# Optimization experiments

Measured on AMD Instinct MI355X. Metric: run time of the kernel, lower is better.

Reference implementation:

```python
import jax, jax.numpy as jnp
import numpy as np

EPS = 1e-5


def mish(x):
    return x * jnp.tanh(jax.nn.softplus(x))


def layer_norm(x, g, b):
    mu = jnp.mean(x, axis=-1, keepdims=True)
    var = jnp.var(x, axis=-1, keepdims=True)
    return (x - mu) / jnp.sqrt(var + EPS) * g + b


def setup_inputs() -> dict:
    key = jax.random.key(0)
    ks = jax.random.split(key, 10)
    D = 256      # hidden_size == encoder feature dim
    L = 64       # max_length
    B, N, K, Q = 2, 10, 1, 5
    NQ = N * Q   # na_rate = 0
    s = 0.02
    inp = {
        "support": jax.random.normal(ks[0], (B * N * K, L, D), jnp.float32),
        "query": jax.random.normal(ks[1], (B * NQ, L, D), jnp.float32),
        "ln_g": jnp.ones((D,), jnp.float32),
        "ln_b": jnp.zeros((D,), jnp.float32),
        "ln2_g": jnp.ones((2 * D,), jnp.float32),
        "ln2_b": jnp.zeros((2 * D,), jnp.float32),
        "proj_W": jax.random.normal(ks[2], (D, 4 * D), jnp.float32) * s,
        "proj_b": jnp.zeros((D,), jnp.float32),
        "W1": jax.random.normal(ks[3], (D, 4 * D), jnp.float32) * s,
        "b1": jnp.zeros((D,), jnp.float32),
        "W2": jax.random.normal(ks[4], (1, D), jnp.float32) * s,
        "b2": jnp.zeros((1,), jnp.float32),
        "W3": jax.random.normal(ks[5], (1, 1), jnp.float32) * s,  # MLP_out Linear(K=1, 1)
        "b3": jnp.zeros((1,), jnp.float32),
        "N": N, "K": K, "Q": Q,
    }
    return inp


def reference(support, query, ln_g, ln_b, ln2_g, ln2_b, proj_W, proj_b,
              W1, b1, W2, b2, W3, b3, N, K, Q):
    L, D = support.shape[-2], support.shape[-1]
    B = support.shape[0] // (N * K)
    NQ = query.shape[0] // B  # = N*Q + na*Q

    s = layer_norm(support, ln_g, ln_b)
    q = layer_norm(query, ln_g, ln_b)

    # expand to all (query, support) pairs: [B, NQ, N*K, L, D] -> [M, L, D]
    s_e = jnp.broadcast_to(s.reshape(B, 1, N * K, L, D), (B, NQ, N * K, L, D)).reshape(-1, L, D)
    q_e = jnp.broadcast_to(q.reshape(B, NQ, 1, L, D), (B, NQ, N * K, L, D)).reshape(-1, L, D)

    # bidirectional cross-attention (no scaling, as in the original)
    att = jnp.einsum('mld,mkd->mlk', s_e, q_e)            # [M, Ls, Lq]
    s_att = jnp.einsum('mlk,mkd->mld', jax.nn.softmax(att, axis=2), q_e)
    q_att = jnp.einsum('mlk,mld->mkd', jax.nn.softmax(att, axis=1), s_e)

    enh_s = jnp.concatenate([s_e, s_att, jnp.abs(s_e - s_att), s_e * s_att], axis=-1)
    enh_q = jnp.concatenate([q_e, q_att, jnp.abs(q_e - q_att), q_e * q_att], axis=-1)
    s_p = mish(enh_s @ proj_W.T + proj_b)
    q_p = mish(enh_q @ proj_W.T + proj_b)

    # pool_norm: max+mean over length, then LayerNorm(2D)
    s_pool = layer_norm(jnp.concatenate([jnp.max(s_p, axis=-2), jnp.mean(s_p, axis=-2)], axis=-1), ln2_g, ln2_b)
    q_pool = layer_norm(jnp.concatenate([jnp.max(q_p, axis=-2), jnp.mean(q_p, axis=-2)], axis=-1), ln2_g, ln2_b)

    cat_seq = jnp.concatenate([q_pool, s_pool], axis=-1)  # [M, 4D]
    h = mish(cat_seq @ W1.T + b1) @ W2.T + b2             # MLProc -> [M, 1]
    logits = mish(h) @ W3.T + b3                          # MLP_out (K=1) -> [M, 1]

    logits = logits.reshape(B, NQ, N)
    minn = jnp.min(logits, axis=-1)
    logits = jnp.concatenate([logits, minn[..., None] - 1.0], axis=2)  # [B, NQ, N+1]
    pred = jnp.argmax(logits.reshape(-1, N + 1), axis=1)
    return logits, pred
```

## Files before the change

### kernel.cpp

```cpp
#include <hip/hip_runtime.h>

typedef unsigned int u32;
typedef unsigned short u16;
#define LN_EPS 1e-5f

typedef __attribute__((ext_vector_type(8))) short short8v;
typedef __attribute__((ext_vector_type(4))) float f32x4;

#define MFMA(acc, a, b) acc = __builtin_amdgcn_mfma_f32_16x16x32_bf16(a, b, acc, 0, 0, 0)

__device__ __forceinline__ float wave_sum(float v){
  #pragma unroll
  for (int o = 32; o > 0; o >>= 1) v += __shfl_xor(v, o, 64);
  return v;
}
__device__ __forceinline__ float mishf(float v){
  float t = __expf(v);
  float u = t*t + 2.f*t;
  return v * (1.f - 2.f/(u + 2.f));
}
__device__ __forceinline__ float bf2f(u16 h){
  return __uint_as_float(((u32)h) << 16);
}
__device__ __forceinline__ u32 pack_split(float x){
  u32 u = __float_as_uint(x);
  u32 h = (u + 0x8000u) & 0xffff0000u;
  float lf = x - __uint_as_float(h);
  return h | (__float_as_uint(lf) >> 16);
}
__device__ __forceinline__ void split_pair(float x0, float x1, u32& hw, u32& lw){
  u32 u0 = __float_as_uint(x0), u1 = __float_as_uint(x1);
  u32 h0 = (u0 + 0x8000u) & 0xffff0000u;
  u32 h1 = (u1 + 0x8000u) & 0xffff0000u;
  float l0 = x0 - __uint_as_float(h0);
  float l1 = x1 - __uint_as_float(h1);
  hw = (h0 >> 16) | h1;
  lw = (__float_as_uint(l0) >> 16) | (__float_as_uint(l1) & 0xffff0000u);
}
__device__ __forceinline__ void split8v(f32x4 a, f32x4 b, short8v& hi, short8v& lo){
  union { short8v v; u32 w[4]; } H, L;
  split_pair(a[0], a[1], H.w[0], L.w[0]);
  split_pair(a[2], a[3], H.w[1], L.w[1]);
  split_pair(b[0], b[1], H.w[2], L.w[2]);
  split_pair(b[2], b[3], H.w[3], L.w[3]);
  hi = H.v; lo = L.v;
}
__device__ __forceinline__ void unpack8(uint4 q0, uint4 q1, short8v& hi, short8v& lo){
  union { short8v v; u32 w[4]; } H, L;
  H.w[0] = (q0.x >> 16) | (q0.y & 0xffff0000u);
  L.w[0] = (q0.x & 0xffffu) | (q0.y << 16);
  H.w[1] = (q0.z >> 16) | (q0.w & 0xffff0000u);
  L.w[1] = (q0.z & 0xffffu) | (q0.w << 16);
  H.w[2] = (q1.x >> 16) | (q1.y & 0xffff0000u);
  L.w[2] = (q1.x & 0xffffu) | (q1.y << 16);
  H.w[3] = (q1.z >> 16) | (q1.w & 0xffff0000u);
  L.w[3] = (q1.z & 0xffffu) | (q1.w << 16);
  hi = H.v; lo = L.v;
}

__global__ void k_setup_ln(const float* __restrict__ sup, const float* __restrict__ qry,
                           const float* __restrict__ lng, const float* __restrict__ lnb,
                           u16* __restrict__ SHI, u16* __restrict__ SLO,
                           u16* __restrict__ QHI, u16* __restrict__ QLO)
{
  const int seq = blockIdx.x;
  const float* src; u16 *dh, *dl;
  if (seq < 20){
    src = sup + (size_t)seq*16384;
    dh = SHI + (size_t)seq*16384; dl = SLO + (size_t)seq*16384;
  } else {
    src = qry + (size_t)(seq-20)*16384;
    dh = QHI + (size_t)(seq-20)*16384; dl = QLO + (size_t)(seq-20)*16384;
  }
  const int t = threadIdx.x, w = t >> 6, lane = t & 63;
  float4 g4 = *(const float4*)(lng + lane*4);
  float4 b4 = *(const float4*)(lnb + lane*4);
  for (int r = w; r < 64; r += 4){
    float4 x = *(const float4*)(src + r*256 + lane*4);
    float s  = wave_sum(x.x + x.y + x.z + x.w);
    float sq = wave_sum(x.x*x.x + x.y*x.y + x.z*x.z + x.w*x.w);
    float mu = s*(1.f/256.f);
    float rstd = 1.f/sqrtf(sq*(1.f/256.f) - mu*mu + LN_EPS);
    float y0 = (x.x - mu)*rstd*g4.x + b4.x;
    float y1 = (x.y - mu)*rstd*g4.y + b4.y;
    float y2 = (x.z - mu)*rstd*g4.z + b4.z;
    float y3 = (x.w - mu)*rstd*g4.w + b4.w;
    u32 p0 = pack_split(y0), p1 = pack_split(y1), p2 = pack_split(y2), p3 = pack_split(y3);
    ushort4 hv = make_ushort4((u16)(p0>>16),(u16)(p1>>16),(u16)(p2>>16),(u16)(p3>>16));
    ushort4 lv = make_ushort4((u16)(p0&0xffffu),(u16)(p1&0xffffu),(u16)(p2&0xffffu),(u16)(p3&0xffffu));
    *(ushort4*)(dh + r*256 + lane*4) = hv;
    *(ushort4*)(dl + r*256 + lane*4) = lv;
  }
}

__global__ void k_setup_w(const float* __restrict__ Wg,
                          u16* __restrict__ WHI, u16* __restrict__ WLO)
{
  const int gid = blockIdx.x*256 + threadIdx.x;
  const int ks = gid >> 10, rem = gid & 1023, nt = rem >> 6, l = rem & 63;
  const int n  = nt*16 + (l & 15);
  const int k0 = ks*32 + (l >> 4)*8;
  const float* src = Wg + n*1024 + k0;
  float4 xa = *(const float4*)src;
  float4 xb = *(const float4*)(src + 4);
  f32x4 fa, fb;
  fa[0]=xa.x; fa[1]=xa.y; fa[2]=xa.z; fa[3]=xa.w;
  fb[0]=xb.x; fb[1]=xb.y; fb[2]=xb.z; fb[3]=xb.w;
  short8v hi, lo;
  split8v(fa, fb, hi, lo);
  *(short8v*)(WHI + (size_t)gid*8) = hi;
  *(short8v*)(WLO + (size_t)gid*8) = lo;
}

__global__ void k_setup_w1t(const float* __restrict__ W1, float* __restrict__ W1T2)
{
  const int gid = blockIdx.x*256 + threadIdx.x;
  const int kb = gid >> 8, n = gid & 255;
  float4 v = *(const float4*)(W1 + n*1024 + kb*4);
  *(float4*)(W1T2 + kb*1024 + n*4) = v;
}

__global__ __launch_bounds__(256) void k_setup_xp(
    const u16* __restrict__ SHI, const u16* __restrict__ SLO,
    const u16* __restrict__ QHI, const u16* __restrict__ QLO,
    const u16* __restrict__ WHI, const u16* __restrict__ WLO,
    float* __restrict__ XPS, float* __restrict__ XPQ)
{
  const int seq = blockIdx.x;
  const u16 *Xh, *Xl; float* out;
  if (seq < 20){
    Xh = SHI + (size_t)seq*16384; Xl = SLO + (size_t)seq*16384;
    out = XPS + (size_t)seq*16384;
  } else {
    Xh = QHI + (size_t)(seq-20)*16384; Xl = QLO + (size_t)(seq-20)*16384;
    out = XPQ + (size_t)(seq-20)*16384;
  }
  const int t = threadIdx.x, w = t >> 6, l = t & 63;
  const int l15 = l & 15, l4 = l >> 4;
  const int Mg = w >> 1, Ng = w & 1;

  f32x4 acc[2][8];
  #pragma unroll
  for (int i = 0; i < 2; i++)
    #pragma unroll
    for (int j = 0; j < 8; j++){ acc[i][j][0]=0.f; acc[i][j][1]=0.f; acc[i][j][2]=0.f; acc[i][j][3]=0.f; }

  for (int ks = 0; ks < 8; ks++){
    short8v ah[2], al[2];
    #pragma unroll
    for (int mt = 0; mt < 2; mt++){
      const int ro = (Mg*32 + mt*16 + l15)*256 + ks*32 + l4*8;
      ah[mt] = *(const short8v*)(Xh + ro);
      al[mt] = *(const short8v*)(Xl + ro);
    }
    #pragma unroll
    for (int nt = 0; nt < 8; nt++){
      const int fo = (ks*16 + Ng*8 + nt)*512 + l*8;
      short8v bh = *(const short8v*)(WHI + fo);
      short8v bl = *(const short8v*)(WLO + fo);
      #pragma unroll
      for (int mt = 0; mt < 2; mt++){
        MFMA(acc[mt][nt], ah[mt], bh);
        MFMA(acc[mt][nt], ah[mt], bl);
        MFMA(acc[mt][nt], al[mt], bh);
      }
    }
  }
  #pragma unroll
  for (int mt = 0; mt < 2; mt++)
    #pragma unroll
    for (int nt = 0; nt < 8; nt++)
      #pragma unroll
      for (int r = 0; r < 4; r++)
        out[(Mg*32 + mt*16 + l4*4 + r)*256 + Ng*128 + nt*16 + l15] = acc[mt][nt][r];
}

#define WLH(BUF, C, H) { const int base_ = (((C)*8 + ch)*16 + Ng*8 + (H)*4)*512 + l*8; \
  _Pragma("unroll") for (int j_ = 0; j_ < 4; j_++){ \
    BUF[j_*2]   = *(const short8v*)(WHI + base_ + j_*512); \
    BUF[j_*2+1] = *(const short8v*)(WLO + base_ + j_*512); } }
#define WMH(BUF, G, H) { _Pragma("unroll") for (int j_ = 0; j_ < 4; j_++){ \
  MFMA(acc[0][(H)*4+j_], fh[G][0], BUF[j_*2]); \
  MFMA(acc[0][(H)*4+j_], fh[G][0], BUF[j_*2+1]); \
  MFMA(acc[0][(H)*4+j_], fl[G][0], BUF[j_*2]); \
  MFMA(acc[1][(H)*4+j_], fh[G][1], BUF[j_*2]); \
  MFMA(acc[1][(H)*4+j_], fh[G][1], BUF[j_*2+1]); \
  MFMA(acc[1][(H)*4+j_], fl[G][1], BUF[j_*2]); } }

__global__ __launch_bounds__(256, 2) void k_pair13(
    const u16* __restrict__ SHI, const u16* __restrict__ SLO,
    const u16* __restrict__ QHI, const u16* __restrict__ QLO,
    const u16* __restrict__ WHI, const u16* __restrict__ WLO,
    const float* __restrict__ XPS, const float* __restrict__ XPQ,
    const float* __restrict__ W1T2,
    const float* __restrict__ pbias,
    const float* __restrict__ ln2g, const float* __restrict__ ln2b,
    const float* __restrict__ b1,
    const float* __restrict__ W2,  const float* __restrict__ b2,
    const float* __restrict__ W3,  const float* __restrict__ b3,
    float* __restrict__ logits)
{
  __shared__ float SM[17296];
  float* S0  = SM;
  u16*   OcT = (u16*)(SM + 4352);
  float* AOc = SM + 9472;
  u32*   P   = (u32*)(SM + 11776);
  float* cat = SM + 16128;
  float* smx = SM + 17152;
  float* smi = SM + 17216;
  float* red = SM + 17280;
  float* stat= SM + 17288;
  float* mred= SM + 17290;

  const int m = (blockIdx.x & 7)*125 + (blockIdx.x >> 3);
  const int b = m / 500, rr = m % 500, nq = rr / 10, n_ = rr % 10;
  const u16* Sh = SHI + (size_t)(b*10 + n_) * 16384;
  const u16* Sl = SLO + (size_t)(b*10 + n_) * 16384;
  const u16* Qh = QHI + (size_t)(b*50 + nq) * 16384;
  const u16* Ql = QLO + (size_t)(b*50 + nq) * 16384;
  const float* xpS = XPS + (size_t)(b*10 + n_) * 16384;
  const float* xpQ = XPQ + (size_t)(b*50 + nq) * 16384;

  const int t = threadIdx.x, w = t >> 6, l = t & 63;
  const int l15 = l & 15, l4 = l >> 4;

  {
    f32x4 acc4[4];
    #pragma unroll
    for (int i = 0; i < 4; i++){ acc4[i][0]=0.f; acc4[i][1]=0.f; acc4[i][2]=0.f; acc4[i][3]=0.f; }
    const u16* Sa = Sh + (w*16+l15)*256 + l4*8;
    const u16* Sb = Sl + (w*16+l15)*256 + l4*8;
    short8v ah = *(const short8v*)Sa;
    short8v al = *(const short8v*)Sb;
    short8v bh[4], bl[4];
    #pragma unroll
    for (int nt = 0; nt < 4; nt++){
      bh[nt] = *(const short8v*)(Qh + (nt*16+l15)*256 + l4*8);
      bl[nt] = *(const short8v*)(Ql + (nt*16+l15)*256 + l4*8);
    }
    #pragma unroll
    for (int ch = 0; ch < 8; ch++){
      short8v nah, nal, nbh[4], nbl[4];
      if (ch < 7){
        nah = *(const short8v*)(Sa + (ch+1)*32);
        nal = *(const short8v*)(Sb + (ch+1)*32);
        #pragma unroll
        for (int nt = 0; nt < 4; nt++){
          nbh[nt] = *(const short8v*)(Qh + (nt*16+l15)*256 + (ch+1)*32 + l4*8);
          nbl[nt] = *(const short8v*)(Ql + (nt*16+l15)*256 + (ch+1)*32 + l4*8);
        }
      }
      #pragma unroll
      for (int nt = 0; nt < 4; nt++){
        MFMA(acc4[nt], ah, bh[nt]);
        MFMA(acc4[nt], ah, bl[nt]);
        MFMA(acc4[nt], al, bh[nt]);
      }
      if (ch < 7){
        ah = nah; al = nal;
        #pragma unroll
        for (int nt = 0; nt < 4; nt++){ bh[nt] = nbh[nt]; bl[nt] = nbl[nt]; }
      }
    }
    #pragma unroll
    for (int nt = 0; nt < 4; nt++)
      #pragma unroll
      for (int r = 0; r < 4; r++)
        S0[(w*16 + l4*4 + r)*68 + nt*16 + l15] = acc4[nt][r];
    __syncthreads();
  }

  auto softmax_row = [&](){
    if (t < 64){
      float mxv = -1e30f, sm = 0.f;
      for (int k = 0; k < 64; k++) mxv = fmaxf(mxv, S0[t*68 + k]);
      for (int k = 0; k < 64; k++) sm += __expf(S0[t*68 + k] - mxv);
      smx[t] = mxv; smi[t] = 1.f/sm;
    }
    __syncthreads();
    #pragma unroll
    for (int r = 0; r < 16; r++){
      int idx = t + 256*r, ll = idx >> 6, k = idx & 63;
      P[ll*68 + k] = pack_split(__expf(S0[ll*68 + k] - smx[ll]) * smi[ll]);
    }
    __syncthreads();
  };
  auto softmax_col_T = [&](){
    if (t < 64){
      float mxv = -1e30f, sm = 0.f;
      for (int ld = 0; ld < 64; ld++) mxv = fmaxf(mxv, S0[ld*68 + t]);
      for (int ld = 0; ld < 64; ld++) sm += __expf(S0[ld*68 + t] - mxv);
      smx[t] = mxv; smi[t] = 1.f/sm;
    }
    __syncthreads();
    #pragma unroll
    for (int r = 0; r < 16; r++){
      int idx = t + 256*r, ll = idx >> 6, k = idx & 63;
      P[k*68 + ll] = pack_split(__expf(S0[ll*68 + k] - smx[k]) * smi[k]);
    }
    __syncthreads();
  };

  auto do_side = [&](const u16* Xh, const u16* Xl, const u16* Oh, const u16* Ol,
                     const float* xp, int cat_off){
    const int Mg = w >> 1, Ng = w & 1;
    f32x4 acc[2][8];
    #pragma unroll
    for (int mt = 0; mt < 2; mt++)
      #pragma unroll
      for (int nt = 0; nt < 8; nt++){
        const float* xr = xp + (Mg*32 + mt*16 + l4*4)*256 + Ng*128 + nt*16 + l15;
        acc[mt][nt][0] = xr[0];
        acc[mt][nt][1] = xr[256];
        acc[mt][nt][2] = xr[512];
        acc[mt][nt][3] = xr[768];
      }

    short8v svh = *(const short8v*)(Oh + l*256 + w*8);
    short8v svl = *(const short8v*)(Ol + l*256 + w*8);
    #pragma unroll
    for (int e = 0; e < 8; e++){
      OcT[(w*8+e)*80 + l]        = (u16)svh[e];
      OcT[2560 + (w*8+e)*80 + l] = (u16)svl[e];
    }
    svh = *(const short8v*)(Oh + l*256 + 32 + w*8);
    svl = *(const short8v*)(Ol + l*256 + 32 + w*8);
    __syncthreads();

    const int xoff = (Mg*32 + l15)*256 + l4*8;

    #pragma unroll 1
    for (int ch = 0; ch < 8; ch++){
      short8v xh0 = *(const short8v*)(Xh + xoff + ch*32);
      short8v xl0 = *(const short8v*)(Xl + xoff + ch*32);
      short8v xh1 = *(const short8v*)(Xh + xoff + 4096 + ch*32);
      short8v xl1 = *(const short8v*)(Xl + xoff + 4096 + ch*32);

      {
        const u16* Ob = OcT + (ch&1)*5120;
        f32x4 ao0 = {0.f,0.f,0.f,0.f}, ao1 = {0.f,0.f,0.f,0.f};
        #pragma unroll
        for (int ks = 0; ks < 2; ks++){
          const u32* pp = P + (w*16 + l15)*68 + ks*32 + l4*8;
          uint4 q0 = *(const uint4*)pp;
          uint4 q1 = *(const uint4*)(pp + 4);
          short8v ph, pl; unpack8(q0, q1, ph, pl);
          const u16* ob0 = Ob + l15*80 + ks*32 + l4*8;
          const u16* ob1 = Ob + (16 + l15)*80 + ks*32 + l4*8;
          short8v bh0 = *(const short8v*)ob0;
          short8v bl0 = *(const short8v*)(ob0 + 2560);
          short8v bh1 = *(const short8v*)ob1;
          short8v bl1 = *(const short8v*)(ob1 + 2560);
          MFMA(ao0, ph, bh0); MFMA(ao0, ph, bl0); MFMA(ao0, pl, bh0);
          MFMA(ao1, ph, bh1); MFMA(ao1, ph, bl1); MFMA(ao1, pl, bh1);
        }
        #pragma unroll
        for (int r = 0; r < 4; r++){
          AOc[(w*16 + l4*4 + r)*36 + l15]      = ao0[r];
          AOc[(w*16 + l4*4 + r)*36 + 16 + l15] = ao1[r];
        }
      }
      __syncthreads();

      if (ch < 7){
        u16* Ob1 = OcT + ((ch+1)&1)*5120;
        #pragma unroll
        for (int e = 0; e < 8; e++){
          Ob1[(w*8+e)*80 + l]        = (u16)svh[e];
          Ob1[2560 + (w*8+e)*80 + l] = (u16)svl[e];
        }
      }
      if (ch < 6){
        svh = *(const short8v*)(Oh + l*256 + (ch+2)*32 + w*8);
        svl = *(const short8v*)(Ol + l*256 + (ch+2)*32 + w*8);
      }

      short8v fh[3][2], fl[3][2];
      {
        f32x4 xv0[2], xv1[2], av0[2], av1[2];
        #pragma unroll
        for (int mt_ = 0; mt_ < 2; mt_++){
          short8v xh = mt_ ? xh1 : xh0;
          short8v xl = mt_ ? xl1 : xl0;
          #pragma unroll
          for (int e_ = 0; e_ < 4; e_++){
            xv0[mt_][e_] = bf2f((u16)xh[e_])     + bf2f((u16)xl[e_]);
            xv1[mt_][e_] = bf2f((u16)xh[4 + e_]) + bf2f((u16)xl[4 + e_]);
          }
          const int row = Mg*32 + mt_*16 + l15;
          av0[mt_] = *(const f32x4*)(AOc + row*36 + l4*8);
          av1[mt_] = *(const f32x4*)(AOc + row*36 + l4*8 + 4);
        }
        #pragma unroll
        for (int mt_ = 0; mt_ < 2; mt_++){
          split8v(av0[mt_], av1[mt_], fh[0][mt_], fl[0][mt_]);
          f32x4 d0, d1, p0, p1;
          #pragma unroll
          for (int e_ = 0; e_ < 4; e_++){
            d0[e_] = fabsf(xv0[mt_][e_] - av0[mt_][e_]);
            d1[e_] = fabsf(xv1[mt_][e_] - av1[mt_][e_]);
            p0[e_] = xv0[mt_][e_] * av0[mt_][e_];
            p1[e_] = xv1[mt_][e_] * av1[mt_][e_];
          }
          split8v(d0, d1, fh[1][mt_], fl[1][mt_]);
          split8v(p0, p1, fh[2][mt_], fl[2][mt_]);
        }
      }

      {
        short8v wa[8], wb[8];
        WLH(wa, 1, 0); WLH(wb, 1, 1);
        WMH(wa, 0, 0);
        WLH(wa, 2, 0);
        WMH(wb, 0, 1);
        WLH(wb, 2, 1);
        WMH(wa, 1, 0);
        WLH(wa, 3, 0);
        WMH(wb, 1, 1);
        WLH(wb, 3, 1);
        WMH(wa, 2, 0);
        WMH(wb, 2, 1);
      }
      __syncthreads();
    }

    float* pmax2 = (float*)P;
    float* psum2 = pmax2 + 512;
    #pragma unroll
    for (int nt = 0; nt < 8; nt++){
      const int col = Ng*128 + nt*16 + l15;
      const float pb = pbias[col];
      float mx = -1e30f, sm = 0.f;
      #pragma unroll
      for (int mt_ = 0; mt_ < 2; mt_++)
        #pragma unroll
        for (int r = 0; r < 4; r++){
          float v = mishf(acc[mt_][nt][r] + pb);
          mx = fmaxf(mx, v); sm += v;
        }
      mx = fmaxf(mx, __shfl_xor(mx, 16, 64));
      mx = fmaxf(mx, __shfl_xor(mx, 32, 64));
      sm += __shfl_xor(sm, 16, 64);
      sm += __shfl_xor(sm, 32, 64);
      if (l4 == 0){ pmax2[Mg*256 + col] = mx; psum2[Mg*256 + col] = sm; }
    }
    __syncthreads();
    float v1 = fmaxf(pmax2[t], pmax2[256 + t]);
    float v2 = (psum2[t] + psum2[256 + t]) * (1.f/64.f);
    float p1 = wave_sum(v1 + v2);
    float p2 = wave_sum(v1*v1 + v2*v2);
    if (l == 0){ red[w] = p1; red[4 + w] = p2; }
    __syncthreads();
    if (t == 0){
      float s1 = red[0]+red[1]+red[2]+red[3];
      float s2 = red[4]+red[5]+red[6]+red[7];
      float mu  = s1 * (1.f/512.f);
      float var = s2 * (1.f/512.f) - mu*mu;
      stat[0] = mu; stat[1] = 1.f/sqrtf(var + LN_EPS);
    }
    __syncthreads();
    float mu = stat[0], rstd = stat[1];
    cat[cat_off + t]       = (v1 - mu)*rstd*ln2g[t]       + ln2b[t];
    cat[cat_off + 256 + t] = (v2 - mu)*rstd*ln2g[256 + t] + ln2b[256 + t];
    __syncthreads();
  };

  softmax_row();
  do_side(Sh, Sl, Qh, Ql, xpS, 512);
  softmax_col_T();
  do_side(Qh, Ql, Sh, Sl, xpQ, 0);

  {
    float acc1 = 0.f;
    const float* wt = W1T2 + t*4;
    #pragma unroll 8
    for (int kb = 0; kb < 256; kb++){
      float4 wv = *(const float4*)(wt + kb*1024);
      const float* cp = &cat[kb*4];
      acc1 += cp[0]*wv.x + cp[1]*wv.y + cp[2]*wv.z + cp[3]*wv.w;
    }
    float hv = mishf(acc1 + b1[t]);
    float contrib = wave_sum(hv * W2[t]);
    if (l == 0) mred[w] = contrib;
  }
  __syncthreads();
  if (t == 0){
    float hh = mred[0] + mred[1] + mred[2] + mred[3] + b2[0];
    logits[m] = mishf(hh)*W3[0] + b3[0];
  }
}

__global__ void k_final9(const float* __restrict__ logits, float* __restrict__ out){
  int t = threadIdx.x;
  if (t < 100){
    float v[10];
    float mn = 1e30f;
    #pragma unroll
    for (int j = 0; j < 10; j++){ v[j] = logits[t*10 + j]; mn = fminf(mn, v[j]); }
    float best = -1e30f; int bi = 0;
    #pragma unroll
    for (int j = 0; j < 10; j++){ if (v[j] > best){ best = v[j]; bi = j; } }
    #pragma unroll
    for (int j = 0; j < 10; j++) out[t*11 + j] = v[j];
    out[t*11 + 10] = mn - 1.f;
    out[1100 + t] = (float)bi;
  }
}

extern "C" void kernel_launch(void* const* d_in, const int* in_sizes, int n_in,
                              void* d_out, int out_size, void* d_ws, size_t ws_size,
                              hipStream_t stream){
  (void)in_sizes; (void)n_in; (void)out_size; (void)ws_size;
  const float* support = (const float*)d_in[0];
  const float* query   = (const float*)d_in[1];
  const float* ln_g    = (const float*)d_in[2];
  const float* ln_b    = (const float*)d_in[3];
  const float* ln2_g   = (const float*)d_in[4];
  const float* ln2_b   = (const float*)d_in[5];
  const float* proj_W  = (const float*)d_in[6];
  const float* proj_b  = (const float*)d_in[7];
  const float* W1      = (const float*)d_in[8];
  const float* b1      = (const float*)d_in[9];
  const float* W2      = (const float*)d_in[10];
  const float* b2      = (const float*)d_in[11];
  const float* W3      = (const float*)d_in[12];
  const float* b3      = (const float*)d_in[13];

  char* wsb = (char*)d_ws;
  float* logits = (float*)wsb;
  u16* SHI = (u16*)(wsb + 4096);
  u16* SLO = SHI + (size_t)20*16384;
  u16* QHI = SLO + (size_t)20*16384;
  u16* QLO = QHI + (size_t)100*16384;
  u16* WHI = QLO + (size_t)100*16384;
  u16* WLO = WHI + (size_t)262144;
  float* XPS  = (float*)(WLO + (size_t)262144);
  float* XPQ  = XPS + (size_t)20*16384;
  float* W1T2 = XPQ + (size_t)100*16384;

  k_setup_ln<<<dim3(120), dim3(256), 0, stream>>>(support, query, ln_g, ln_b,
                                                  SHI, SLO, QHI, QLO);
  k_setup_w<<<dim3(128), dim3(256), 0, stream>>>(proj_W, WHI, WLO);
  k_setup_w1t<<<dim3(256), dim3(256), 0, stream>>>(W1, W1T2);
  k_setup_xp<<<dim3(120), dim3(256), 0, stream>>>(SHI, SLO, QHI, QLO, WHI, WLO,
                                                  XPS, XPQ);
  k_pair13<<<dim3(1000), dim3(256), 0, stream>>>(SHI, SLO, QHI, QLO, WHI, WLO,
                                                 XPS, XPQ, W1T2,
                                                 proj_b, ln2_g, ln2_b,
                                                 b1, W2, b2, W3, b3, logits);
  k_final9<<<dim3(1), dim3(128), 0, stream>>>(logits, (float*)d_out);
}
```

Before: 399.9 us.

## Merge setup kernels and double-buffer attention output to drop a barrier per chunk

Fuses the three setup kernels (LayerNorm split, proj weight split, W1 transpose) into one launch with block-index dispatch. In the main pair kernel, the attention-output staging buffer becomes double-buffered in shared memory. This lets one __syncthreads per chunk be removed and moves the first weight-fragment load earlier so it overlaps the attention MFMA work. The cost is more shared memory per block, which may reduce occupancy, and a longer live range for the weight registers.

Result: no change. 395.5 us, median of 3 (-1.1%).

```diff
diff --git a/kernel.cpp b/kernel.cpp
--- a/kernel.cpp
+++ b/kernel.cpp
@@ -58,66 +58,66 @@
   hi = H.v; lo = L.v;
 }
 
-__global__ void k_setup_ln(const float* __restrict__ sup, const float* __restrict__ qry,
-                           const float* __restrict__ lng, const float* __restrict__ lnb,
-                           u16* __restrict__ SHI, u16* __restrict__ SLO,
-                           u16* __restrict__ QHI, u16* __restrict__ QLO)
+__global__ void k_setup_A(const float* __restrict__ sup, const float* __restrict__ qry,
+                          const float* __restrict__ lng, const float* __restrict__ lnb,
+                          const float* __restrict__ Wg,  const float* __restrict__ W1,
+                          u16* __restrict__ SHI, u16* __restrict__ SLO,
+                          u16* __restrict__ QHI, u16* __restrict__ QLO,
+                          u16* __restrict__ WHI, u16* __restrict__ WLO,
+                          float* __restrict__ W1T2)
 {
-  const int seq = blockIdx.x;
-  const float* src; u16 *dh, *dl;
-  if (seq < 20){
-    src = sup + (size_t)seq*16384;
-    dh = SHI + (size_t)seq*16384; dl = SLO + (size_t)seq*16384;
+  const int bid = blockIdx.x, t = threadIdx.x;
+
+  if (bid < 120){
+    const int seq = bid;
+    const float* src; u16 *dh, *dl;
+    if (seq < 20){
+      src = sup + (size_t)seq*16384;
+      dh = SHI + (size_t)seq*16384; dl = SLO + (size_t)seq*16384;
+    } else {
+      src = qry + (size_t)(seq-20)*16384;
+      dh = QHI + (size_t)(seq-20)*16384; dl = QLO + (size_t)(seq-20)*16384;
+    }
+    const int w = t >> 6, lane = t & 63;
+    float4 g4 = *(const float4*)(lng + lane*4);
+    float4 b4 = *(const float4*)(lnb + lane*4);
+    for (int r = w; r < 64; r += 4){
+      float4 x = *(const float4*)(src + r*256 + lane*4);
+      float s  = wave_sum(x.x + x.y + x.z + x.w);
+      float sq = wave_sum(x.x*x.x + x.y*x.y + x.z*x.z + x.w*x.w);
+      float mu = s*(1.f/256.f);
+      float rstd = 1.f/sqrtf(sq*(1.f/256.f) - mu*mu + LN_EPS);
+      float y0 = (x.x - mu)*rstd*g4.x + b4.x;
+      float y1 = (x.y - mu)*rstd*g4.y + b4.y;
+      float y2 = (x.z - mu)*rstd*g4.z + b4.z;
+      float y3 = (x.w - mu)*rstd*g4.w + b4.w;
+      u32 p0 = pack_split(y0), p1 = pack_split(y1), p2 = pack_split(y2), p3 = pack_split(y3);
+      ushort4 hv = make_ushort4((u16)(p0>>16),(u16)(p1>>16),(u16)(p2>>16),(u16)(p3>>16));
+      ushort4 lv = make_ushort4((u16)(p0&0xffffu),(u16)(p1&0xffffu),(u16)(p2&0xffffu),(u16)(p3&0xffffu));
+      *(ushort4*)(dh + r*256 + lane*4) = hv;
+      *(ushort4*)(dl + r*256 + lane*4) = lv;
+    }
+  } else if (bid < 248){
+    const int gid = (bid-120)*256 + t;
+    const int ks = gid >> 10, rem = gid & 1023, nt = rem >> 6, l = rem & 63;
+    const int n  = nt*16 + (l & 15);
+    const int k0 = ks*32 + (l >> 4)*8;
+    const float* src = Wg + n*1024 + k0;
+    float4 xa = *(const float4*)src;
+    float4 xb = *(const float4*)(src + 4);
+    f32x4 fa, fb;
+    fa[0]=xa.x; fa[1]=xa.y; fa[2]=xa.z; fa[3]=xa.w;
+    fb[0]=xb.x; fb[1]=xb.y; fb[2]=xb.z; fb[3]=xb.w;
+    short8v hi, lo;
+    split8v(fa, fb, hi, lo);
+    *(short8v*)(WHI + (size_t)gid*8) = hi;
+    *(short8v*)(WLO + (size_t)gid*8) = lo;
   } else {
-    src = qry + (size_t)(seq-20)*16384;
-    dh = QHI + (size_t)(seq-20)*16384; dl = QLO + (size_t)(seq-20)*16384;
-  }
-  const int t = threadIdx.x, w = t >> 6, lane = t & 63;
-  float4 g4 = *(const float4*)(lng + lane*4);
-  float4 b4 = *(const float4*)(lnb + lane*4);
-  for (int r = w; r < 64; r += 4){
-    float4 x = *(const float4*)(src + r*256 + lane*4);
-    float s  = wave_sum(x.x + x.y + x.z + x.w);
-    float sq = wave_sum(x.x*x.x + x.y*x.y + x.z*x.z + x.w*x.w);
-    float mu = s*(1.f/256.f);
-    float rstd = 1.f/sqrtf(sq*(1.f/256.f) - mu*mu + LN_EPS);
-    float y0 = (x.x - mu)*rstd*g4.x + b4.x;
-    float y1 = (x.y - mu)*rstd*g4.y + b4.y;
-    float y2 = (x.z - mu)*rstd*g4.z + b4.z;
-    float y3 = (x.w - mu)*rstd*g4.w + b4.w;
-    u32 p0 = pack_split(y0), p1 = pack_split(y1), p2 = pack_split(y2), p3 = pack_split(y3);
-    ushort4 hv = make_ushort4((u16)(p0>>16),(u16)(p1>>16),(u16)(p2>>16),(u16)(p3>>16));
-    ushort4 lv = make_ushort4((u16)(p0&0xffffu),(u16)(p1&0xffffu),(u16)(p2&0xffffu),(u16)(p3&0xffffu));
-    *(ushort4*)(dh + r*256 + lane*4) = hv;
-    *(ushort4*)(dl + r*256 + lane*4) = lv;
-  }
-}
-
-__global__ void k_setup_w(const float* __restrict__ Wg,
-                          u16* __restrict__ WHI, u16* __restrict__ WLO)
-{
-  const int gid = blockIdx.x*256 + threadIdx.x;
-  const int ks = gid >> 10, rem = gid & 1023, nt = rem >> 6, l = rem & 63;
-  const int n  = nt*16 + (l & 15);
-  const int k0 = ks*32 + (l >> 4)*8;
-  const float* src = Wg + n*1024 + k0;
-  float4 xa = *(const float4*)src;
-  float4 xb = *(const float4*)(src + 4);
-  f32x4 fa, fb;
-  fa[0]=xa.x; fa[1]=xa.y; fa[2]=xa.z; fa[3]=xa.w;
-  fb[0]=xb.x; fb[1]=xb.y; fb[2]=xb.z; fb[3]=xb.w;
-  short8v hi, lo;
-  split8v(fa, fb, hi, lo);
-  *(short8v*)(WHI + (size_t)gid*8) = hi;
-  *(short8v*)(WLO + (size_t)gid*8) = lo;
-}
-
-__global__ void k_setup_w1t(const float* __restrict__ W1, float* __restrict__ W1T2)
-{
-  const int gid = blockIdx.x*256 + threadIdx.x;
-  const int kb = gid >> 8, n = gid & 255;
-  float4 v = *(const float4*)(W1 + n*1024 + kb*4);
-  *(float4*)(W1T2 + kb*1024 + n*4) = v;
+    const int gid = (bid-248)*256 + t;
+    const int kb = gid >> 8, n = gid & 255;
+    float4 v = *(const float4*)(W1 + n*1024 + kb*4);
+    *(float4*)(W1T2 + kb*1024 + n*4) = v;
+  }
 }
 
 __global__ __launch_bounds__(256) void k_setup_xp(
@@ -187,7 +187,7 @@
   MFMA(acc[1][(H)*4+j_], fh[G][1], BUF[j_*2+1]); \
   MFMA(acc[1][(H)*4+j_], fl[G][1], BUF[j_*2]); } }
 
-__global__ __launch_bounds__(256, 2) void k_pair13(
+__global__ __launch_bounds__(256, 2) void k_pair15(
     const u16* __restrict__ SHI, const u16* __restrict__ SLO,
     const u16* __restrict__ QHI, const u16* __restrict__ QLO,
     const u16* __restrict__ WHI, const u16* __restrict__ WLO,
@@ -200,17 +200,17 @@
     const float* __restrict__ W3,  const float* __restrict__ b3,
     float* __restrict__ logits)
 {
-  __shared__ float SM[17296];
+  __shared__ float SM[19600];
   float* S0  = SM;
   u16*   OcT = (u16*)(SM + 4352);
   float* AOc = SM + 9472;
-  u32*   P   = (u32*)(SM + 11776);
-  float* cat = SM + 16128;
-  float* smx = SM + 17152;
-  float* smi = SM + 17216;
-  float* red = SM + 17280;
-  float* stat= SM + 17288;
-  float* mred= SM + 17290;
+  u32*   P   = (u32*)(SM + 14080);
+  float* cat = SM + 18432;
+  float* smx = SM + 19456;
+  float* smi = SM + 19520;
+  float* red = SM + 19584;
+  float* stat= SM + 19592;
+  float* mred= SM + 19594;
 
   const int m = (blockIdx.x & 7)*125 + (blockIdx.x >> 3);
   const int b = m / 500, rr = m % 500, nq = rr / 10, n_ = rr % 10;
@@ -335,6 +335,8 @@
       short8v xl0 = *(const short8v*)(Xl + xoff + ch*32);
       short8v xh1 = *(const short8v*)(Xh + xoff + 4096 + ch*32);
       short8v xl1 = *(const short8v*)(Xl + xoff + 4096 + ch*32);
+      short8v wa[8], wb[8];
+      WLH(wa, 1, 0);
 
       {
         const u16* Ob = OcT + (ch&1)*5120;
@@ -354,13 +356,13 @@
           MFMA(ao0, ph, bh0); MFMA(ao0, ph, bl0); MFMA(ao0, pl, bh0);
           MFMA(ao1, ph, bh1); MFMA(ao1, ph, bl1); MFMA(ao1, pl, bh1);
         }
+        float* Ad = AOc + (ch&1)*2304;
         #pragma unroll
         for (int r = 0; r < 4; r++){
-          AOc[(w*16 + l4*4 + r)*36 + l15]      = ao0[r];
-          AOc[(w*16 + l4*4 + r)*36 + 16 + l15] = ao1[r];
-        }
-      }
-      __syncthreads();
+          Ad[(w*16 + l4*4 + r)*36 + l15]      = ao0[r];
+          Ad[(w*16 + l4*4 + r)*36 + 16 + l15] = ao1[r];
+        }
+      }
 
       if (ch < 7){
         u16* Ob1 = OcT + ((ch+1)&1)*5120;
@@ -374,9 +376,11 @@
         svh = *(const short8v*)(Oh + l*256 + (ch+2)*32 + w*8);
         svl = *(const short8v*)(Ol + l*256 + (ch+2)*32 + w*8);
       }
+      __syncthreads();
 
       short8v fh[3][2], fl[3][2];
       {
+        const float* Ad = AOc + (ch&1)*2304;
         f32x4 xv0[2], xv1[2], av0[2], av1[2];
         #pragma unroll
         for (int mt_ = 0; mt_ < 2; mt_++){
@@ -388,8 +392,8 @@
             xv1[mt_][e_] = bf2f((u16)xh[4 + e_]) + bf2f((u16)xl[4 + e_]);
           }
           const int row = Mg*32 + mt_*16 + l15;
-          av0[mt_] = *(const f32x4*)(AOc + row*36 + l4*8);
-          av1[mt_] = *(const f32x4*)(AOc + row*36 + l4*8 + 4);
+          av0[mt_] = *(const f32x4*)(Ad + row*36 + l4*8);
+          av1[mt_] = *(const f32x4*)(Ad + row*36 + l4*8 + 4);
         }
         #pragma unroll
         for (int mt_ = 0; mt_ < 2; mt_++){
@@ -407,21 +411,17 @@
         }
       }
 
-      {
-        short8v wa[8], wb[8];
-        WLH(wa, 1, 0); WLH(wb, 1, 1);
-        WMH(wa, 0, 0);
-        WLH(wa, 2, 0);
-        WMH(wb, 0, 1);
-        WLH(wb, 2, 1);
-        WMH(wa, 1, 0);
-        WLH(wa, 3, 0);
-        WMH(wb, 1, 1);
-        WLH(wb, 3, 1);
-        WMH(wa, 2, 0);
-        WMH(wb, 2, 1);
-      }
-      __syncthreads();
+      WLH(wb, 1, 1);
+      WMH(wa, 0, 0);
+      WLH(wa, 2, 0);
+      WMH(wb, 0, 1);
+      WLH(wb, 2, 1);
+      WMH(wa, 1, 0);
+      WLH(wa, 3, 0);
+      WMH(wb, 1, 1);
+      WLH(wb, 3, 1);
+      WMH(wa, 2, 0);
+      WMH(wb, 2, 1);
     }
 
     float* pmax2 = (float*)P;
@@ -538,13 +538,13 @@
   float* XPQ  = XPS + (size_t)20*16384;
   float* W1T2 = XPQ + (size_t)100*16384;
 
-  k_setup_ln<<<dim3(120), dim3(256), 0, stream>>>(support, query, ln_g, ln_b,
-                                                  SHI, SLO, QHI, QLO);
-  k_setup_w<<<dim3(128), dim3(256), 0, stream>>>(proj_W, WHI, WLO);
-  k_setup_w1t<<<dim3(256), dim3(256), 0, stream>>>(W1, W1T2);
+  k_setup_A<<<dim3(504), dim3(256), 0, stream>>>(support, query, ln_g, ln_b,
+                                                 proj_W, W1,
+                                                 SHI, SLO, QHI, QLO, WHI, WLO,
+                                                 W1T2);
   k_setup_xp<<<dim3(120), dim3(256), 0, stream>>>(SHI, SLO, QHI, QLO, WHI, WLO,
                                                   XPS, XPQ);
-  k_pair13<<<dim3(1000), dim3(256), 0, stream>>>(SHI, SLO, QHI, QLO, WHI, WLO,
+  k_pair15<<<dim3(1000), dim3(256), 0, stream>>>(SHI, SLO, QHI, QLO, WHI, WLO,
                                                  XPS, XPQ, W1T2,
                                                  proj_b, ln2_g, ln2_b,
                                                  b1, W2, b2, W3, b3, logits);
```
